# Performance work log

Measured on AMD Instinct MI355X. Metric: run time of the kernel, lower is better.

## Reference

```python
import jax, jax.numpy as jnp
import numpy as np

B, T, E, HD = 8, 2048, 1024, 64  # batch, seq (== n_ctx), n_embd, head_dim = n_embd // n_head


def setup_inputs() -> dict:
    key = jax.random.key(0)
    k1, k2, k3, k4 = jax.random.split(key, 4)
    x = jax.random.normal(k1, (B, T, E), dtype=jnp.float32)
    s = E ** -0.5  # Linear-like init scale
    Wq = jax.random.normal(k2, (E, HD), dtype=jnp.float32) * s
    Wk = jax.random.normal(k3, (E, HD), dtype=jnp.float32) * s
    Wv = jax.random.normal(k4, (E, HD), dtype=jnp.float32) * s
    return {"x": x, "Wq": Wq, "Wk": Wk, "Wv": Wv}


def reference(x, Wq, Wk, Wv):
    # q,k,v: [B, T, HD]
    q = jnp.einsum('bte,eh->bth', x, Wq)
    k = jnp.einsum('bte,eh->bth', x, Wk)
    v = jnp.einsum('bte,eh->bth', x, Wv)
    scale = k.shape[-1] ** -0.5
    # scores: [B, T, T]
    alpha = jnp.einsum('bqh,bkh->bqk', q, k) * scale
    causal = jnp.tril(jnp.ones((T, T), dtype=bool))
    alpha = jnp.where(causal, alpha, -jnp.inf)
    alpha = jax.nn.softmax(alpha, axis=-1)
    # dropout with p=0.0 is identity in eval
    h = jnp.einsum('bqk,bkh->bqh', alpha, v)  # [B, T, HD]
    return h
```

## Files before the change

kernel.cpp:

```cpp
#include <hip/hip_runtime.h>
#include <hip/hip_bf16.h>
#include <math.h>

#define BATCH 8
#define T 2048
#define E 1024
#define HD 64
#define BT (BATCH * T)

typedef __bf16 bf16_t;
typedef bf16_t bf16x4 __attribute__((ext_vector_type(4)));
typedef bf16_t bf16x8 __attribute__((ext_vector_type(8)));
typedef float f32x4 __attribute__((ext_vector_type(4)));

#define MFMA(a, b, c) __builtin_amdgcn_mfma_f32_16x16x32_bf16((a), (b), (c), 0, 0, 0)

#define QSCALE (0.125f * 1.44269504088896340736f)


__global__ __launch_bounds__(256) void prep_w(const float* __restrict__ Wq,
                                              const float* __restrict__ Wk,
                                              const float* __restrict__ Wv,
                                              bf16_t* __restrict__ WTt) {
    const int nt  = blockIdx.x >> 3;
    const int kc0 = (blockIdx.x & 7) * 128;
    const int tid = threadIdx.x;
    const int l16 = tid & 15;
    const int k8  = (kc0 >> 3) + (tid >> 4);
    const int n   = nt * 16 + l16;
    const int m   = n >> 6;
    const int col = n & 63;
    const float* W = (m == 0) ? Wq : (m == 1) ? Wk : Wv;
    const float scale = (m == 0) ? QSCALE : 1.0f;
    bf16x8 o;
#pragma unroll
    for (int j = 0; j < 8; j++) {
        o[j] = (bf16_t)(W[(size_t)(k8 * 8 + j) * HD + col] * scale);
    }
    *reinterpret_cast<bf16x8*>(WTt + (size_t)nt * 16384 + k8 * 128 + l16 * 8) = o;
}

__global__ __launch_bounds__(256, 4) void qkv_proj(
    const float* __restrict__ x,
    const bf16_t* __restrict__ WTt,
    bf16_t* __restrict__ qt,
    bf16_t* __restrict__ kt,
    bf16_t* __restrict__ vt)
{
    __shared__ __align__(16) bf16_t xbuf[2][16][72];

    const int tid  = threadIdx.x;
    const int wave = tid >> 6;
    const int lane = tid & 63;
    const int l16  = lane & 15;
    const int quad = lane >> 4;
    const int rowbase0 = blockIdx.x * 16;

    const int srow = tid >> 4;
    const int sseg = tid & 15;
    const float* xsrc = x + (size_t)(rowbase0 + srow) * E + sseg * 4;

    const bf16_t* Bb = WTt + (size_t)(wave * 3) * 16384 + lane * 8;

    f32x4 acc[3] = {};

    {
        const f32x4 xa = *reinterpret_cast<const f32x4*>(xsrc);
        bf16x4 xw;
#pragma unroll
        for (int u = 0; u < 4; u++) xw[u] = (bf16_t)xa[u];
        *reinterpret_cast<bf16x4*>(&xbuf[0][srow][sseg * 4]) = xw;
    }
    bf16x8 bcur[2][3];
#pragma unroll
    for (int ks = 0; ks < 2; ks++) {
#pragma unroll
        for (int tc = 0; tc < 3; tc++) {
            bcur[ks][tc] = *reinterpret_cast<const bf16x8*>(
                Bb + (size_t)tc * 16384 + (ks * 32) * 16);
        }
    }
    __syncthreads();

    int p = 0;
    for (int kc = 0; kc < E; kc += 64) {
        const int kn = (kc + 64) & (E - 1);
        const f32x4 nxa = *reinterpret_cast<const f32x4*>(xsrc + kn);
        bf16x8 bn[2][3];
#pragma unroll
        for (int ks = 0; ks < 2; ks++) {
#pragma unroll
            for (int tc = 0; tc < 3; tc++) {
                bn[ks][tc] = *reinterpret_cast<const bf16x8*>(
                    Bb + (size_t)tc * 16384 + (kn + ks * 32) * 16);
            }
        }

        const bf16x8 a0 = *reinterpret_cast<const bf16x8*>(&xbuf[p][l16][quad * 8]);
        const bf16x8 a1 = *reinterpret_cast<const bf16x8*>(&xbuf[p][l16][32 + quad * 8]);

#pragma unroll
        for (int tc = 0; tc < 3; tc++) acc[tc] = MFMA(a0, bcur[0][tc], acc[tc]);
#pragma unroll
        for (int tc = 0; tc < 3; tc++) acc[tc] = MFMA(a1, bcur[1][tc], acc[tc]);

        bf16x4 xw;
#pragma unroll
        for (int u = 0; u < 4; u++) xw[u] = (bf16_t)nxa[u];
        *reinterpret_cast<bf16x4*>(&xbuf[p ^ 1][srow][sseg * 4]) = xw;
        __syncthreads();
        p ^= 1;

#pragma unroll
        for (int ks = 0; ks < 2; ks++) {
#pragma unroll
            for (int tc = 0; tc < 3; tc++) bcur[ks][tc] = bn[ks][tc];
        }
    }

    const int rowbase = rowbase0;
#pragma unroll
    for (int tc = 0; tc < 3; tc++) {
        const int n0  = wave * 48 + tc * 16;
        const int m   = n0 >> 6;
        const int tcg = (n0 & 63) >> 4;
        if (m < 2) {
            bf16_t* dst = (m == 0) ? qt : kt;
            const size_t o0 = (size_t)(rowbase >> 4) * 1024 +
                              (size_t)(tcg * 2 + (l16 >> 3)) * 128 + (l16 & 7);
#pragma unroll
            for (int r = 0; r < 4; r++) {
                dst[o0 + (quad * 4 + r) * 8] = (bf16_t)acc[tc][r];
            }
        } else {
            const int b_    = rowbase >> 11;
            const int tbase = rowbase & (T - 1);
            const size_t o0 = (size_t)b_ * 131072 +
                              (size_t)((tbase >> 3) + (quad >> 1)) * 128 +
                              l16 * 8 + (quad & 1) * 4 + (size_t)tcg * 32768;
            bf16x4 pv;
#pragma unroll
            for (int r = 0; r < 4; r++) pv[r] = (bf16_t)acc[tc][r];
            *reinterpret_cast<bf16x4*>(vt + o0) = pv;
        }
    }
}

__global__ __launch_bounds__(512, 2) void attn(
    const bf16_t* __restrict__ qtl,
    const bf16_t* __restrict__ ktl,
    const bf16_t* __restrict__ vtl,
    float* __restrict__ out)
{
    __shared__ __align__(16) bf16_t plds[8][16][40];
    __shared__ float opart[8][16][66];
    __shared__ float lpart[8][16];

    const int wave = threadIdx.x >> 6;
    const int lane = threadIdx.x & 63;
    const int l16  = lane & 15;
    const int quad = lane >> 4;
    const int group = wave >> 2;
    const int kw    = wave & 3;

    const int b  = blockIdx.x >> 6;
    const int pr = blockIdx.x & 63;
    const int qt = group ? (127 - pr) : pr;
    const int rowbase = qt * 16;

    const bf16_t* Qb = qtl + (size_t)((b * T + rowbase) >> 4) * 1024 + lane * 8;
    const bf16_t* Kb = ktl + (size_t)b * T * 64 + lane * 8;
    const bf16_t* Vb = vtl + (size_t)b * 131072 + lane * 8;

    const bf16x8 qf0 = *reinterpret_cast<const bf16x8*>(Qb);
    const bf16x8 qf1 = *reinterpret_cast<const bf16x8*>(Qb + 512);

    f32x4 o[4] = {};
    f32x4 lrun = {};

    const int nch = (rowbase + 47) >> 5;

    int k0 = kw * 32;
    bf16x8 kfa0 = *reinterpret_cast<const bf16x8*>(Kb + k0 * 64);
    bf16x8 kfb0 = *reinterpret_cast<const bf16x8*>(Kb + k0 * 64 + 512);
    bf16x8 kfa1 = *reinterpret_cast<const bf16x8*>(Kb + k0 * 64 + 1024);
    bf16x8 kfb1 = *reinterpret_cast<const bf16x8*>(Kb + k0 * 64 + 1536);
    bf16x8 vf0 = *reinterpret_cast<const bf16x8*>(Vb + k0 * 16);
    bf16x8 vf1 = *reinterpret_cast<const bf16x8*>(Vb + k0 * 16 + 32768);
    bf16x8 vf2 = *reinterpret_cast<const bf16x8*>(Vb + k0 * 16 + 65536);
    bf16x8 vf3 = *reinterpret_cast<const bf16x8*>(Vb + k0 * 16 + 98304);

    for (int c = kw; c < nch; c += 4) {
        k0 = c * 32;
        const int cn = (c + 4 < nch) ? (c + 4) : c;
        const int kn = cn * 32;
        bf16x8 nkfa0 = *reinterpret_cast<const bf16x8*>(Kb + kn * 64);
        bf16x8 nkfb0 = *reinterpret_cast<const bf16x8*>(Kb + kn * 64 + 512);
        bf16x8 nkfa1 = *reinterpret_cast<const bf16x8*>(Kb + kn * 64 + 1024);
        bf16x8 nkfb1 = *reinterpret_cast<const bf16x8*>(Kb + kn * 64 + 1536);
        bf16x8 nvf0 = *reinterpret_cast<const bf16x8*>(Vb + kn * 16);
        bf16x8 nvf1 = *reinterpret_cast<const bf16x8*>(Vb + kn * 16 + 32768);
        bf16x8 nvf2 = *reinterpret_cast<const bf16x8*>(Vb + kn * 16 + 65536);
        bf16x8 nvf3 = *reinterpret_cast<const bf16x8*>(Vb + kn * 16 + 98304);

        f32x4 s_lo = {};
        f32x4 s_hi = {};
        s_lo = MFMA(qf0, kfa0, s_lo);
        s_lo = MFMA(qf1, kfb0, s_lo);
        s_hi = MFMA(qf0, kfa1, s_hi);
        s_hi = MFMA(qf1, kfb1, s_hi);

        if (k0 + 31 > rowbase) {
            const int row = rowbase + quad * 4;
#pragma unroll
            for (int r = 0; r < 4; r++) {
                if (k0 + l16 > row + r)      s_lo[r] = -INFINITY;
                if (k0 + 16 + l16 > row + r) s_hi[r] = -INFINITY;
            }
        }

#pragma unroll
        for (int r = 0; r < 4; r++) {
            const float p0 = exp2f(s_lo[r]);
            const float p1 = exp2f(s_hi[r]);
            lrun[r] += p0 + p1;
            plds[wave][quad * 4 + r][l16]      = (bf16_t)p0;
            plds[wave][quad * 4 + r][16 + l16] = (bf16_t)p1;
        }
        const bf16x8 pf = *reinterpret_cast<const bf16x8*>(&plds[wave][l16][quad * 8]);

        o[0] = MFMA(pf, vf0, o[0]);
        o[1] = MFMA(pf, vf1, o[1]);
        o[2] = MFMA(pf, vf2, o[2]);
        o[3] = MFMA(pf, vf3, o[3]);

        kfa0 = nkfa0; kfb0 = nkfb0; kfa1 = nkfa1; kfb1 = nkfb1;
        vf0 = nvf0; vf1 = nvf1; vf2 = nvf2; vf3 = nvf3;
    }

#pragma unroll
    for (int r = 0; r < 4; r++) {
        float l = lrun[r];
        l += __shfl_xor(l, 1);
        l += __shfl_xor(l, 2);
        l += __shfl_xor(l, 4);
        l += __shfl_xor(l, 8);
        if (l16 == 0) lpart[wave][quad * 4 + r] = l;
#pragma unroll
        for (int nb = 0; nb < 4; nb++) {
            opart[wave][quad * 4 + r][nb * 16 + l16] = o[nb][r];
        }
    }
    __syncthreads();

    const int g    = threadIdx.x >> 8;
    const int gtid = threadIdx.x & 255;
    const int qtg  = g ? (127 - pr) : pr;
    const size_t outbase = (size_t)b * T + qtg * 16;
#pragma unroll
    for (int pass = 0; pass < 4; pass++) {
        const int row = pass * 4 + (gtid >> 6);
        const int col = gtid & 63;
        float osum = 0.f, lsum = 0.f;
#pragma unroll
        for (int w = 0; w < 4; w++) {
            osum += opart[g * 4 + w][row][col];
            lsum += lpart[g * 4 + w][row];
        }
        out[(outbase + row) * HD + col] = osum / lsum;
    }
}

extern "C" void kernel_launch(void* const* d_in, const int* in_sizes, int n_in,
                              void* d_out, int out_size, void* d_ws, size_t ws_size,
                              hipStream_t stream) {
    const float* x  = (const float*)d_in[0];
    const float* Wq = (const float*)d_in[1];
    const float* Wk = (const float*)d_in[2];
    const float* Wv = (const float*)d_in[3];
    float* out = (float*)d_out;

    bf16_t* ws  = (bf16_t*)d_ws;
    bf16_t* WTt = ws;
    bf16_t* qtl = WTt + (size_t)192 * E;
    bf16_t* ktl = qtl + (size_t)BT * HD;
    bf16_t* vtl = ktl + (size_t)BT * HD;

    prep_w<<<96, 256, 0, stream>>>(Wq, Wk, Wv, WTt);
    qkv_proj<<<1024, 256, 0, stream>>>(x, WTt, qtl, ktl, vtl);
    attn<<<512, 512, 0, stream>>>(qtl, ktl, vtl, out);
}
```

Before: 132.7 us.

## Stage full x row tile into LDS via async global_load_lds with XOR swizzle

The QKV projection kernel now loads the whole 16x1024 fp32 x tile into LDS at once using direct global-to-LDS loads with an XOR swizzle. This replaces the per-iteration register-staged, double-buffered bf16 copy, and it removes the per-iteration __syncthreads and the software prefetch of weights. The fp32-to-bf16 conversion now happens after the LDS read. LDS use rises to 64 KB per block, so the occupancy hint drops from 4 to 2. The kernel loses overlap between loading x and computing, and weight loads are no longer prefetched.

Measured after the change: 124.1 us. 1.07x faster.

```diff
diff --git a/kernel.cpp b/kernel.cpp
--- a/kernel.cpp
+++ b/kernel.cpp
@@ -40,14 +40,14 @@
     *reinterpret_cast<bf16x8*>(WTt + (size_t)nt * 16384 + k8 * 128 + l16 * 8) = o;
 }
 
-__global__ __launch_bounds__(256, 4) void qkv_proj(
+__global__ __launch_bounds__(256, 2) void qkv_proj(
     const float* __restrict__ x,
     const bf16_t* __restrict__ WTt,
     bf16_t* __restrict__ qt,
     bf16_t* __restrict__ kt,
     bf16_t* __restrict__ vt)
 {
-    __shared__ __align__(16) bf16_t xbuf[2][16][72];
+    __shared__ __align__(16) float xlds[16][1024];
 
     const int tid  = threadIdx.x;
     const int wave = tid >> 6;
@@ -56,66 +56,53 @@
     const int quad = lane >> 4;
     const int rowbase0 = blockIdx.x * 16;
 
-    const int srow = tid >> 4;
-    const int sseg = tid & 15;
-    const float* xsrc = x + (size_t)(rowbase0 + srow) * E + sseg * 4;
-
     const bf16_t* Bb = WTt + (size_t)(wave * 3) * 16384 + lane * 8;
 
     f32x4 acc[3] = {};
 
-    {
-        const f32x4 xa = *reinterpret_cast<const f32x4*>(xsrc);
-        bf16x4 xw;
-#pragma unroll
-        for (int u = 0; u < 4; u++) xw[u] = (bf16_t)xa[u];
-        *reinterpret_cast<bf16x4*>(&xbuf[0][srow][sseg * 4]) = xw;
-    }
-    bf16x8 bcur[2][3];
-#pragma unroll
-    for (int ks = 0; ks < 2; ks++) {
-#pragma unroll
-        for (int tc = 0; tc < 3; tc++) {
-            bcur[ks][tc] = *reinterpret_cast<const bf16x8*>(
-                Bb + (size_t)tc * 16384 + (ks * 32) * 16);
-        }
+#pragma unroll
+    for (int i = 0; i < 16; i++) {
+        const int r  = wave * 4 + (i >> 2);
+        const int qq = i & 3;
+        const float* gsrc = x + (size_t)(rowbase0 + r) * E + qq * 256 +
+                            ((lane ^ (r & 7)) * 4);
+        __builtin_amdgcn_global_load_lds(
+            (const __attribute__((address_space(1))) unsigned int*)gsrc,
+            (__attribute__((address_space(3))) unsigned int*)&xlds[r][qq * 256],
+            16, 0, 0);
     }
     __syncthreads();
 
-    int p = 0;
     for (int kc = 0; kc < E; kc += 64) {
-        const int kn = (kc + 64) & (E - 1);
-        const f32x4 nxa = *reinterpret_cast<const f32x4*>(xsrc + kn);
-        bf16x8 bn[2][3];
+        bf16x8 bf[2][3];
 #pragma unroll
         for (int ks = 0; ks < 2; ks++) {
 #pragma unroll
             for (int tc = 0; tc < 3; tc++) {
-                bn[ks][tc] = *reinterpret_cast<const bf16x8*>(
-                    Bb + (size_t)tc * 16384 + (kn + ks * 32) * 16);
+                bf[ks][tc] = *reinterpret_cast<const bf16x8*>(
+                    Bb + (size_t)tc * 16384 + (kc + ks * 32) * 16);
             }
         }
 
-        const bf16x8 a0 = *reinterpret_cast<const bf16x8*>(&xbuf[p][l16][quad * 8]);
-        const bf16x8 a1 = *reinterpret_cast<const bf16x8*>(&xbuf[p][l16][32 + quad * 8]);
-
-#pragma unroll
-        for (int tc = 0; tc < 3; tc++) acc[tc] = MFMA(a0, bcur[0][tc], acc[tc]);
-#pragma unroll
-        for (int tc = 0; tc < 3; tc++) acc[tc] = MFMA(a1, bcur[1][tc], acc[tc]);
-
-        bf16x4 xw;
-#pragma unroll
-        for (int u = 0; u < 4; u++) xw[u] = (bf16_t)nxa[u];
-        *reinterpret_cast<bf16x4*>(&xbuf[p ^ 1][srow][sseg * 4]) = xw;
-        __syncthreads();
-        p ^= 1;
-
-#pragma unroll
-        for (int ks = 0; ks < 2; ks++) {
-#pragma unroll
-            for (int tc = 0; tc < 3; tc++) bcur[ks][tc] = bn[ks][tc];
-        }
+        const int rx = l16 & 7;
+        const int c0 = (kc >> 2) + quad * 2;
+        const f32x4 va0 = *reinterpret_cast<const f32x4*>(&xlds[l16][((c0)     ^ rx) * 4]);
+        const f32x4 vb0 = *reinterpret_cast<const f32x4*>(&xlds[l16][((c0 + 1) ^ rx) * 4]);
+        const f32x4 va1 = *reinterpret_cast<const f32x4*>(&xlds[l16][((c0 + 8) ^ rx) * 4]);
+        const f32x4 vb1 = *reinterpret_cast<const f32x4*>(&xlds[l16][((c0 + 9) ^ rx) * 4]);
+        bf16x8 a0, a1;
+#pragma unroll
+        for (int u = 0; u < 4; u++) {
+            a0[u]     = (bf16_t)va0[u];
+            a0[4 + u] = (bf16_t)vb0[u];
+            a1[u]     = (bf16_t)va1[u];
+            a1[4 + u] = (bf16_t)vb1[u];
+        }
+
+#pragma unroll
+        for (int tc = 0; tc < 3; tc++) acc[tc] = MFMA(a0, bf[0][tc], acc[tc]);
+#pragma unroll
+        for (int tc = 0; tc < 3; tc++) acc[tc] = MFMA(a1, bf[1][tc], acc[tc]);
     }
 
     const int rowbase = rowbase0;
```
